# Kernel tuning notes

Hardware: AMD Instinct MI355X
Metric: run time of the kernel (lower is better)

## Reference

```python
import math
import jax, jax.numpy as jnp
import numpy as np

B = 128          # batch_size (graphs)
SEQ = 128        # max_seq_len (nodes per graph)
D = 128          # input_dim
HID = 64         # enc_hidden_dim
HEADS = 4        # in_head
N = B * SEQ      # total nodes
E = 262144       # edges (avg degree 16)


def _make_pe(seq, d):
    pos = np.arange(seq, dtype=np.float32)[:, None]
    i_even = np.arange(0, d, 2, dtype=np.float32)
    pe = np.zeros((seq, d), dtype=np.float32)
    pe[:, 0::2] = np.sin(pos / 10000.0 ** (2.0 * i_even / d))
    pe[:, 1::2] = np.cos(pos / 10000.0 ** (2.0 * (i_even + 1.0) / d))
    return jnp.asarray(pe)


def setup_inputs() -> dict:
    key = jax.random.key(0)
    ks = jax.random.split(key, 10)
    s = 0.1
    return {
        "x": jax.random.normal(ks[0], (N, D), jnp.float32),
        "edge_index": jax.random.randint(ks[1], (2, E), 0, N),
        "pe": _make_pe(SEQ, D),
        "W1": jax.random.normal(ks[2], (D, HEADS * HID), jnp.float32) * s,
        "a_src1": jax.random.normal(ks[3], (HEADS, HID), jnp.float32) * s,
        "a_dst1": jax.random.normal(ks[4], (HEADS, HID), jnp.float32) * s,
        "b1": jnp.zeros((HEADS * HID,), jnp.float32),
        "W2": jax.random.normal(ks[5], (HEADS * HID, HID), jnp.float32) * s,
        "a_src2": jax.random.normal(ks[6], (1, HID), jnp.float32) * s,
        "a_dst2": jax.random.normal(ks[7], (1, HID), jnp.float32) * s,
        "b2": jnp.zeros((HID,), jnp.float32),
        "batch_size": B,
    }


def _gat_conv(x, src, dst, W, a_src, a_dst, b, heads, ch, concat, n):
    # PyG GATConv (eval mode, self-loops already appended to src/dst).
    h = (x @ W).reshape(n, heads, ch)                      # [N,H,C]
    alpha_src = jnp.einsum("nhc,hc->nh", h, a_src)         # [N,H]
    alpha_dst = jnp.einsum("nhc,hc->nh", h, a_dst)
    e = jax.nn.leaky_relu(alpha_src[src] + alpha_dst[dst], 0.2)  # [E,H]
    m = jax.ops.segment_max(e, dst, num_segments=n)        # segment softmax over dst
    ex = jnp.exp(e - m[dst])
    den = jax.ops.segment_sum(ex, dst, num_segments=n)
    alpha = ex / (den[dst] + 1e-16)                        # [E,H]
    out = jax.ops.segment_sum(h[src] * alpha[:, :, None], dst, num_segments=n)
    out = out.reshape(n, heads * ch) if concat else out.mean(axis=1)
    return out + b


def reference(x, edge_index, pe, W1, a_src1, a_dst1, b1, W2, a_src2, a_dst2, b2, batch_size):
    n = x.shape[0]
    loop = jnp.arange(n)
    src = jnp.concatenate([edge_index[0], loop])           # add self-loops (PyG default)
    dst = jnp.concatenate([edge_index[1], loop])
    # positional encoding (dropout inactive in eval)
    h = x * math.sqrt(x.shape[1]) + jnp.tile(pe, (batch_size, 1))
    h = jax.nn.elu(_gat_conv(h, src, dst, W1, a_src1, a_dst1, b1, HEADS, HID, True, n))
    out = _gat_conv(h, src, dst, W2, a_src2, a_dst2, b2, 1, HID, False, n)
    return out.reshape(batch_size, -1, out.shape[1])
```

## Files before the change

### kernel.cpp

```cpp
#include <hip/hip_runtime.h>
#include <hip/hip_bf16.h>

typedef __hip_bfloat16 bf16;

#define N_NODES 16384
#define D_IN    128
#define HID     64
#define HEADS   4
#define F1      256
#define SEQ     128
#define SLOTS   64

__device__ __forceinline__ float wave_sum(float v) {
    #pragma unroll
    for (int o = 32; o > 0; o >>= 1) v += __shfl_xor(v, o, 64);
    return v;
}
__device__ __forceinline__ float lrelu(float v) { return v > 0.f ? v : 0.2f * v; }
__device__ __forceinline__ float rdlane(float v, int l) {
    return __uint_as_float(__builtin_amdgcn_readlane(__float_as_uint(v), l));
}

#define UNPACK8(u, te, acc)                                          \
    do {                                                             \
        acc[0] += (te) * __uint_as_float((u).x << 16);               \
        acc[1] += (te) * __uint_as_float((u).x & 0xffff0000u);       \
        acc[2] += (te) * __uint_as_float((u).y << 16);               \
        acc[3] += (te) * __uint_as_float((u).y & 0xffff0000u);       \
        acc[4] += (te) * __uint_as_float((u).z << 16);               \
        acc[5] += (te) * __uint_as_float((u).z & 0xffff0000u);       \
        acc[6] += (te) * __uint_as_float((u).w << 16);               \
        acc[7] += (te) * __uint_as_float((u).w & 0xffff0000u);       \
    } while (0)

__global__ __launch_bounds__(256) void k_gemm1s(const float* __restrict__ x,
                                                const float* __restrict__ pe,
                                                const float* __restrict__ W1,
                                                const float* __restrict__ a_src1,
                                                const float* __restrict__ a_dst1,
                                                bf16* __restrict__ h,
                                                float* __restrict__ as1,
                                                float* __restrict__ ad1,
                                                const int* __restrict__ ei, int E, int Etot,
                                                int* __restrict__ cnt,
                                                int* __restrict__ esrc) {
    __shared__ float4 ws[2048];
    int tid = threadIdx.x, lane = tid & 63, wv = tid >> 6;

    {
        int gtid = blockIdx.x * 256 + tid;
        for (int e = gtid; e < Etot; e += 262144) {
            int s, d;
            if (e < E) { s = ei[e]; d = ei[E + e]; }
            else       { s = e - E; d = s; }
            int pos = atomicAdd(&cnt[d], 1);
            if (pos < SLOTS) esrc[d * SLOTS + pos] = s;
        }
    }

    int base = blockIdx.x * 16;
    int j4 = lane * 4;
    float2 xr[4];
    #pragma unroll
    for (int i = 0; i < 4; i++) {
        int row = base + wv * 4 + i;
        float2 xa  = *(const float2*)(x  + (size_t)row * 128 + 2 * lane);
        float2 pea = *(const float2*)(pe + (size_t)(row & (SEQ - 1)) * 128 + 2 * lane);
        xr[i].x = xa.x * 11.313708499f + pea.x;
        xr[i].y = xa.y * 11.313708499f + pea.y;
    }
    float acc[4][4] = {};
    const float4* Wv = (const float4*)W1;
    for (int c = 0; c < 4; c++) {
        if (c > 0) __syncthreads();
        const float4* src = Wv + (size_t)c * 2048;
        #pragma unroll
        for (int i = 0; i < 8; i++) ws[i * 256 + tid] = src[i * 256 + tid];
        __syncthreads();
        #pragma unroll 4
        for (int lk2 = 0; lk2 < 16; lk2++) {
            int k2 = c * 16 + lk2;
            float4 w0 = ws[(2 * lk2) * 64 + lane];
            float4 w1 = ws[(2 * lk2 + 1) * 64 + lane];
            #pragma unroll
            for (int i = 0; i < 4; i++) {
                float a0 = rdlane(xr[i].x, k2);
                float a1 = rdlane(xr[i].y, k2);
                acc[i][0] += a0 * w0.x + a1 * w1.x;
                acc[i][1] += a0 * w0.y + a1 * w1.y;
                acc[i][2] += a0 * w0.z + a1 * w1.z;
                acc[i][3] += a0 * w0.w + a1 * w1.w;
            }
        }
    }
    float4 asv = *(const float4*)(a_src1 + j4);
    float4 adv = *(const float4*)(a_dst1 + j4);
    #pragma unroll
    for (int i = 0; i < 4; i++) {
        int row = base + wv * 4 + i;
        union { bf16 b[4]; ushort4 u; } cv;
        cv.b[0] = __float2bfloat16(acc[i][0]);
        cv.b[1] = __float2bfloat16(acc[i][1]);
        cv.b[2] = __float2bfloat16(acc[i][2]);
        cv.b[3] = __float2bfloat16(acc[i][3]);
        *(ushort4*)(h + (size_t)row * 256 + j4) = cv.u;
        float vs = acc[i][0] * asv.x + acc[i][1] * asv.y + acc[i][2] * asv.z + acc[i][3] * asv.w;
        float vd = acc[i][0] * adv.x + acc[i][1] * adv.y + acc[i][2] * adv.z + acc[i][3] * adv.w;
        #pragma unroll
        for (int o = 1; o < 16; o <<= 1) {
            vs += __shfl_xor(vs, o);
            vd += __shfl_xor(vd, o);
        }
        if ((lane & 15) == 0) {
            as1[row * 4 + (lane >> 4)] = vs;
            ad1[row * 4 + (lane >> 4)] = vd;
        }
    }
}

__global__ __launch_bounds__(256) void k_agg1_gemm2(
        const int* __restrict__ cnt, const int* __restrict__ esrc,
        const float* __restrict__ as1, const float* __restrict__ ad1,
        const bf16* __restrict__ h,
        const float* __restrict__ b1,
        const float* __restrict__ W2,
        const float* __restrict__ a_src2, const float* __restrict__ a_dst2,
        bf16* __restrict__ h2, float* __restrict__ as2, float* __restrict__ ad2) {
    __shared__ float hs[4][256];
    __shared__ float scr[1024];
    __shared__ int   ss[4][64];
    int tid = threadIdx.x, lane = tid & 63, wv = tid >> 6;
    int dbase = blockIdx.x * 4;
    int eg = lane >> 3;
    int cg_ = lane & 7;
    const bf16* hbase = h + (size_t)wv * 64 + cg_ * 8;

    int cv4 = cnt[dbase + (lane & 3)];

    #pragma unroll 4
    for (int it = 0; it < 4; it++) {
        int d = dbase + it;
        int deg = min(__shfl(cv4, it), SLOTS);
        int s = esrc[(size_t)d * SLOTS + lane] & (N_NODES - 1);
        float av = as1[(size_t)s * 4 + wv];
        float adw = ad1[d * 4 + wv];
        float t = (lane < deg) ? __expf(lrelu(av + adw) - 40.f) : 0.f;
        float inv = 1.f / wave_sum(t);
        scr[(it * 4 + wv) * 64 + lane] = t * inv;
        ss[it][lane] = s;
    }

    #pragma unroll 2
    for (int it = 0; it < 4; it++) {
        int deg = min(__shfl(cv4, it), SLOTS);
        const float* tsr = &scr[(it * 4 + wv) * 64];

        float acc[8] = {0, 0, 0, 0, 0, 0, 0, 0};
        if (4 * eg < deg) {
            int4   sv = *(const int4*)&ss[it][4 * eg];
            float4 tv = *(const float4*)(tsr + 4 * eg);
            uint4 u0 = *(const uint4*)(hbase + (size_t)sv.x * 256);
            uint4 u1 = *(const uint4*)(hbase + (size_t)sv.y * 256);
            uint4 u2 = *(const uint4*)(hbase + (size_t)sv.z * 256);
            uint4 u3 = *(const uint4*)(hbase + (size_t)sv.w * 256);
            UNPACK8(u0, tv.x, acc);
            UNPACK8(u1, tv.y, acc);
            UNPACK8(u2, tv.z, acc);
            UNPACK8(u3, tv.w, acc);
        }
        for (int sub = 32; sub < deg; sub += 32) {
            if (sub + 4 * eg < deg) {
                int4   s2 = *(const int4*)&ss[it][sub + 4 * eg];
                float4 t2 = *(const float4*)(tsr + sub + 4 * eg);
                uint4 u0 = *(const uint4*)(hbase + (size_t)s2.x * 256);
                uint4 u1 = *(const uint4*)(hbase + (size_t)s2.y * 256);
                uint4 u2 = *(const uint4*)(hbase + (size_t)s2.z * 256);
                uint4 u3 = *(const uint4*)(hbase + (size_t)s2.w * 256);
                UNPACK8(u0, t2.x, acc);
                UNPACK8(u1, t2.y, acc);
                UNPACK8(u2, t2.z, acc);
                UNPACK8(u3, t2.w, acc);
            }
        }
        #pragma unroll
        for (int j = 0; j < 8; j++) {
            acc[j] += __shfl_xor(acc[j], 8);
            acc[j] += __shfl_xor(acc[j], 16);
            acc[j] += __shfl_xor(acc[j], 32);
        }
        if (lane < 8) {
            int cbase = wv * 64 + lane * 8;
            const float4* b1v = (const float4*)(b1 + cbase);
            float4 bb0 = b1v[0], bb1 = b1v[1];
            float o[8];
            o[0] = acc[0] + bb0.x; o[1] = acc[1] + bb0.y;
            o[2] = acc[2] + bb0.z; o[3] = acc[3] + bb0.w;
            o[4] = acc[4] + bb1.x; o[5] = acc[5] + bb1.y;
            o[6] = acc[6] + bb1.z; o[7] = acc[7] + bb1.w;
            #pragma unroll
            for (int j = 0; j < 8; j++)
                o[j] = o[j] > 0.f ? o[j] : (__expf(o[j]) - 1.f);
            float4* dst = (float4*)&hs[it][cbase];
            dst[0] = make_float4(o[0], o[1], o[2], o[3]);
            dst[1] = make_float4(o[4], o[5], o[6], o[7]);
        }
    }
    __syncthreads();

    {
        float acc2[4] = {0, 0, 0, 0};
        const int k4base = wv * 16;
        for (int kk = 0; kk < 16; kk++) {
            int k4 = k4base + kk;
            const float* wp = W2 + (size_t)k4 * 256 + lane;
            float w0 = wp[0], w1 = wp[64], w2 = wp[128], w3 = wp[192];
            #pragma unroll
            for (int r = 0; r < 4; r++) {
                float4 u = *(const float4*)&hs[r][k4 * 4];
                acc2[r] += u.x * w0 + u.y * w1 + u.z * w2 + u.w * w3;
            }
        }
        #pragma unroll
        for (int r = 0; r < 4; r++) scr[(wv * 4 + r) * 64 + lane] = acc2[r];
    }
    __syncthreads();
    {
        int r = wv;
        float a0 = scr[(0 * 4 + r) * 64 + lane] + scr[(1 * 4 + r) * 64 + lane]
                 + scr[(2 * 4 + r) * 64 + lane] + scr[(3 * 4 + r) * 64 + lane];
        float asj = a_src2[lane], adj = a_dst2[lane];
        int n0 = dbase + r;
        h2[(size_t)n0 * 64 + lane] = __float2bfloat16(a0);
        float va0 = wave_sum(a0 * asj);
        float vd0 = wave_sum(a0 * adj);
        if (lane == 0) {
            as2[n0] = va0; ad2[n0] = vd0;
        }
    }
}

__global__ __launch_bounds__(256) void k_agg2(const int* __restrict__ cnt,
                                              const int* __restrict__ esrc,
                                              const float* __restrict__ as2,
                                              const float* __restrict__ ad2,
                                              const bf16* __restrict__ h2,
                                              const float* __restrict__ b2v,
                                              float* __restrict__ out) {
    __shared__ float ts[4][64];
    int tid = threadIdx.x, lane = tid & 63, wv = tid >> 6;
    int d = blockIdx.x * 4 + wv;
    int deg = min(cnt[d], SLOTS);
    int eg = lane >> 3, cg_ = lane & 7;
    const bf16* hbase = h2 + cg_ * 8;
    const int4* ep4 = (const int4*)(esrc + (size_t)d * SLOTS);

    int4 sv = ep4[eg];
    sv.x &= N_NODES - 1; sv.y &= N_NODES - 1;
    sv.z &= N_NODES - 1; sv.w &= N_NODES - 1;

    int s = esrc[(size_t)d * SLOTS + lane] & (N_NODES - 1);
    float av = as2[s];
    float adw = ad2[d];
    float t = (lane < deg) ? __expf(lrelu(av + adw) - 40.f) : 0.f;
    float inv = 1.f / wave_sum(t);
    ts[wv][lane] = t * inv;

    float acc[8] = {0, 0, 0, 0, 0, 0, 0, 0};
    if (4 * eg < deg) {
        uint4 u0 = *(const uint4*)(hbase + (size_t)sv.x * 64);
        uint4 u1 = *(const uint4*)(hbase + (size_t)sv.y * 64);
        uint4 u2 = *(const uint4*)(hbase + (size_t)sv.z * 64);
        uint4 u3 = *(const uint4*)(hbase + (size_t)sv.w * 64);
        float4 tv = *(const float4*)&ts[wv][4 * eg];
        UNPACK8(u0, tv.x, acc);
        UNPACK8(u1, tv.y, acc);
        UNPACK8(u2, tv.z, acc);
        UNPACK8(u3, tv.w, acc);
    }
    for (int sub = 32; sub < deg; sub += 32) {
        int4 s2 = ep4[(sub >> 2) + eg];
        s2.x &= N_NODES - 1; s2.y &= N_NODES - 1;
        s2.z &= N_NODES - 1; s2.w &= N_NODES - 1;
        if (sub + 4 * eg < deg) {
            uint4 u0 = *(const uint4*)(hbase + (size_t)s2.x * 64);
            uint4 u1 = *(const uint4*)(hbase + (size_t)s2.y * 64);
            uint4 u2 = *(const uint4*)(hbase + (size_t)s2.z * 64);
            uint4 u3 = *(const uint4*)(hbase + (size_t)s2.w * 64);
            float4 t2 = *(const float4*)&ts[wv][sub + 4 * eg];
            UNPACK8(u0, t2.x, acc);
            UNPACK8(u1, t2.y, acc);
            UNPACK8(u2, t2.z, acc);
            UNPACK8(u3, t2.w, acc);
        }
    }
    #pragma unroll
    for (int j = 0; j < 8; j++) {
        acc[j] += __shfl_xor(acc[j], 8);
        acc[j] += __shfl_xor(acc[j], 16);
        acc[j] += __shfl_xor(acc[j], 32);
    }
    if (lane < 8) {
        int cbase = lane * 8;
        float o[8];
        #pragma unroll
        for (int j = 0; j < 8; j++) o[j] = acc[j] + b2v[cbase + j];
        float4* dst = (float4*)(out + (size_t)d * 64 + cbase);
        dst[0] = make_float4(o[0], o[1], o[2], o[3]);
        dst[1] = make_float4(o[4], o[5], o[6], o[7]);
    }
}

extern "C" void kernel_launch(void* const* d_in, const int* in_sizes, int n_in,
                              void* d_out, int out_size, void* d_ws, size_t ws_size,
                              hipStream_t stream) {
    const float* x    = (const float*)d_in[0];
    const int*   ei   = (const int*)  d_in[1];
    const float* pe   = (const float*)d_in[2];
    const float* W1   = (const float*)d_in[3];
    const float* a_s1 = (const float*)d_in[4];
    const float* a_d1 = (const float*)d_in[5];
    const float* b1   = (const float*)d_in[6];
    const float* W2   = (const float*)d_in[7];
    const float* a_s2 = (const float*)d_in[8];
    const float* a_d2 = (const float*)d_in[9];
    const float* b2   = (const float*)d_in[10];

    const int E    = in_sizes[1] / 2;
    const int n    = N_NODES;
    const int Etot = E + n;

    char* p = (char*)d_ws;
    auto alloc = [&](size_t bytes) -> void* {
        void* r = (void*)p;
        p += (bytes + 255) & ~(size_t)255;
        return r;
    };
    int*   cnt     = (int*)  alloc((size_t)n * 4);
    int*   esrc    = (int*)  alloc((size_t)n * SLOTS * 4);
    bf16*  h       = (bf16*) alloc((size_t)n * F1 * 2);
    float* as1     = (float*)alloc((size_t)n * HEADS * 4);
    float* ad1     = (float*)alloc((size_t)n * HEADS * 4);
    bf16*  h2      = (bf16*) alloc((size_t)n * HID * 2);
    float* as2     = (float*)alloc((size_t)n * 4);
    float* ad2     = (float*)alloc((size_t)n * 4);

    hipMemsetAsync(cnt, 0, (size_t)n * 4, stream);

    k_gemm1s    <<<n / 16, 256, 0, stream>>>(x, pe, W1, a_s1, a_d1, h, as1, ad1,
                                             ei, E, Etot, cnt, esrc);
    k_agg1_gemm2<<<n / 4, 256, 0, stream>>>(cnt, esrc, as1, ad1, h, b1,
                                            W2, a_s2, a_d2, h2, as2, ad2);
    k_agg2      <<<n / 4, 256, 0, stream>>>(cnt, esrc, as2, ad2, h2, b2, (float*)d_out);
}
```

Baseline: 170.8 us.

## Switch GAT aggregation to lane-per-channel gathers with packed src/weight pairs in LDS

Both aggregation kernels are restructured. Previously 8 edge groups each loaded 16-byte bf16 vectors and combined results with a cross-lane shuffle reduction. Now each lane owns one channel and walks the edge list serially, loading one bf16 per edge with the next loads prefetched ahead. Source indices and softmax weights are packed as int2 in shared memory so one ds read yields both, and the shuffle reductions plus lane<8 writeback are removed. The trade is many narrow 2-byte gathers in a serial per-wave loop instead of wide parallel vector loads, which could hurt memory efficiency.

```diff
diff --git a/kernel.cpp b/kernel.cpp
--- a/kernel.cpp
+++ b/kernel.cpp
@@ -20,18 +20,9 @@
 __device__ __forceinline__ float rdlane(float v, int l) {
     return __uint_as_float(__builtin_amdgcn_readlane(__float_as_uint(v), l));
 }
-
-#define UNPACK8(u, te, acc)                                          \
-    do {                                                             \
-        acc[0] += (te) * __uint_as_float((u).x << 16);               \
-        acc[1] += (te) * __uint_as_float((u).x & 0xffff0000u);       \
-        acc[2] += (te) * __uint_as_float((u).y << 16);               \
-        acc[3] += (te) * __uint_as_float((u).y & 0xffff0000u);       \
-        acc[4] += (te) * __uint_as_float((u).z << 16);               \
-        acc[5] += (te) * __uint_as_float((u).z & 0xffff0000u);       \
-        acc[6] += (te) * __uint_as_float((u).w << 16);               \
-        acc[7] += (te) * __uint_as_float((u).w & 0xffff0000u);       \
-    } while (0)
+__device__ __forceinline__ float bfu(unsigned short u) {
+    return __uint_as_float((unsigned)u << 16);
+}
 
 __global__ __launch_bounds__(256) void k_gemm1s(const float* __restrict__ x,
                                                 const float* __restrict__ pe,
@@ -127,17 +118,13 @@
         const float* __restrict__ a_src2, const float* __restrict__ a_dst2,
         bf16* __restrict__ h2, float* __restrict__ as2, float* __restrict__ ad2) {
     __shared__ float hs[4][256];
-    __shared__ float scr[1024];
-    __shared__ int   ss[4][64];
+    __shared__ int2  sts[16][64];
     int tid = threadIdx.x, lane = tid & 63, wv = tid >> 6;
     int dbase = blockIdx.x * 4;
-    int eg = lane >> 3;
-    int cg_ = lane & 7;
-    const bf16* hbase = h + (size_t)wv * 64 + cg_ * 8;
 
     int cv4 = cnt[dbase + (lane & 3)];
 
-    #pragma unroll 4
+    #pragma unroll
     for (int it = 0; it < 4; it++) {
         int d = dbase + it;
         int deg = min(__shfl(cv4, it), SLOTS);
@@ -146,66 +133,47 @@
         float adw = ad1[d * 4 + wv];
         float t = (lane < deg) ? __expf(lrelu(av + adw) - 40.f) : 0.f;
         float inv = 1.f / wave_sum(t);
-        scr[(it * 4 + wv) * 64 + lane] = t * inv;
-        ss[it][lane] = s;
-    }
-
+        int2 pr; pr.x = s; pr.y = __float_as_int(t * inv);
+        sts[it * 4 + wv][lane] = pr;
+    }
+
+    const unsigned short* hb = (const unsigned short*)h + (size_t)wv * 64 + lane;
+    float bb = b1[wv * 64 + lane];
     #pragma unroll 2
     for (int it = 0; it < 4; it++) {
         int deg = min(__shfl(cv4, it), SLOTS);
-        const float* tsr = &scr[(it * 4 + wv) * 64];
-
-        float acc[8] = {0, 0, 0, 0, 0, 0, 0, 0};
-        if (4 * eg < deg) {
-            int4   sv = *(const int4*)&ss[it][4 * eg];
-            float4 tv = *(const float4*)(tsr + 4 * eg);
-            uint4 u0 = *(const uint4*)(hbase + (size_t)sv.x * 256);
-            uint4 u1 = *(const uint4*)(hbase + (size_t)sv.y * 256);
-            uint4 u2 = *(const uint4*)(hbase + (size_t)sv.z * 256);
-            uint4 u3 = *(const uint4*)(hbase + (size_t)sv.w * 256);
-            UNPACK8(u0, tv.x, acc);
-            UNPACK8(u1, tv.y, acc);
-            UNPACK8(u2, tv.z, acc);
-            UNPACK8(u3, tv.w, acc);
-        }
-        for (int sub = 32; sub < deg; sub += 32) {
-            if (sub + 4 * eg < deg) {
-                int4   s2 = *(const int4*)&ss[it][sub + 4 * eg];
-                float4 t2 = *(const float4*)(tsr + sub + 4 * eg);
-                uint4 u0 = *(const uint4*)(hbase + (size_t)s2.x * 256);
-                uint4 u1 = *(const uint4*)(hbase + (size_t)s2.y * 256);
-                uint4 u2 = *(const uint4*)(hbase + (size_t)s2.z * 256);
-                uint4 u3 = *(const uint4*)(hbase + (size_t)s2.w * 256);
-                UNPACK8(u0, t2.x, acc);
-                UNPACK8(u1, t2.y, acc);
-                UNPACK8(u2, t2.z, acc);
-                UNPACK8(u3, t2.w, acc);
-            }
-        }
-        #pragma unroll
-        for (int j = 0; j < 8; j++) {
-            acc[j] += __shfl_xor(acc[j], 8);
-            acc[j] += __shfl_xor(acc[j], 16);
-            acc[j] += __shfl_xor(acc[j], 32);
-        }
-        if (lane < 8) {
-            int cbase = wv * 64 + lane * 8;
-            const float4* b1v = (const float4*)(b1 + cbase);
-            float4 bb0 = b1v[0], bb1 = b1v[1];
-            float o[8];
-            o[0] = acc[0] + bb0.x; o[1] = acc[1] + bb0.y;
-            o[2] = acc[2] + bb0.z; o[3] = acc[3] + bb0.w;
-            o[4] = acc[4] + bb1.x; o[5] = acc[5] + bb1.y;
-            o[6] = acc[6] + bb1.z; o[7] = acc[7] + bb1.w;
-            #pragma unroll
-            for (int j = 0; j < 8; j++)
-                o[j] = o[j] > 0.f ? o[j] : (__expf(o[j]) - 1.f);
-            float4* dst = (float4*)&hs[it][cbase];
-            dst[0] = make_float4(o[0], o[1], o[2], o[3]);
-            dst[1] = make_float4(o[4], o[5], o[6], o[7]);
-        }
+        const int4* row4 = (const int4*)sts[it * 4 + wv];
+        int nq = (deg + 3) >> 2;
+        float acc = 0.f;
+        int4 A = row4[0];
+        int4 B = row4[1];
+        unsigned short e0 = hb[(size_t)A.x * 256];
+        unsigned short e1 = hb[(size_t)A.z * 256];
+        unsigned short e2 = hb[(size_t)B.x * 256];
+        unsigned short e3 = hb[(size_t)B.z * 256];
+        for (int q = 1; q < nq; q++) {
+            int4 An = row4[2 * q];
+            int4 Bn = row4[2 * q + 1];
+            unsigned short f0 = hb[(size_t)An.x * 256];
+            unsigned short f1 = hb[(size_t)An.z * 256];
+            unsigned short f2 = hb[(size_t)Bn.x * 256];
+            unsigned short f3 = hb[(size_t)Bn.z * 256];
+            acc += bfu(e0) * __uint_as_float(A.y);
+            acc += bfu(e1) * __uint_as_float(A.w);
+            acc += bfu(e2) * __uint_as_float(B.y);
+            acc += bfu(e3) * __uint_as_float(B.w);
+            A = An; B = Bn; e0 = f0; e1 = f1; e2 = f2; e3 = f3;
+        }
+        acc += bfu(e0) * __uint_as_float(A.y);
+        acc += bfu(e1) * __uint_as_float(A.w);
+        acc += bfu(e2) * __uint_as_float(B.y);
+        acc += bfu(e3) * __uint_as_float(B.w);
+        float v = acc + bb;
+        hs[it][wv * 64 + lane] = v > 0.f ? v : (__expf(v) - 1.f);
     }
     __syncthreads();
+
+    float* part = (float*)sts;
 
     {
         float acc2[4] = {0, 0, 0, 0};
@@ -221,13 +189,13 @@
             }
         }
         #pragma unroll
-        for (int r = 0; r < 4; r++) scr[(wv * 4 + r) * 64 + lane] = acc2[r];
+        for (int r = 0; r < 4; r++) part[(wv * 4 + r) * 64 + lane] = acc2[r];
     }
     __syncthreads();
     {
         int r = wv;
-        float a0 = scr[(0 * 4 + r) * 64 + lane] + scr[(1 * 4 + r) * 64 + lane]
-                 + scr[(2 * 4 + r) * 64 + lane] + scr[(3 * 4 + r) * 64 + lane];
+        float a0 = part[(0 * 4 + r) * 64 + lane] + part[(1 * 4 + r) * 64 + lane]
+                 + part[(2 * 4 + r) * 64 + lane] + part[(3 * 4 + r) * 64 + lane];
         float asj = a_src2[lane], adj = a_dst2[lane];
         int n0 = dbase + r;
         h2[(size_t)n0 * 64 + lane] = __float2bfloat16(a0);
@@ -246,68 +214,47 @@
                                               const bf16* __restrict__ h2,
                                               const float* __restrict__ b2v,
                                               float* __restrict__ out) {
-    __shared__ float ts[4][64];
+    __shared__ int2 sts2[4][64];
     int tid = threadIdx.x, lane = tid & 63, wv = tid >> 6;
     int d = blockIdx.x * 4 + wv;
     int deg = min(cnt[d], SLOTS);
-    int eg = lane >> 3, cg_ = lane & 7;
-    const bf16* hbase = h2 + cg_ * 8;
-    const int4* ep4 = (const int4*)(esrc + (size_t)d * SLOTS);
-
-    int4 sv = ep4[eg];
-    sv.x &= N_NODES - 1; sv.y &= N_NODES - 1;
-    sv.z &= N_NODES - 1; sv.w &= N_NODES - 1;
 
     int s = esrc[(size_t)d * SLOTS + lane] & (N_NODES - 1);
     float av = as2[s];
     float adw = ad2[d];
     float t = (lane < deg) ? __expf(lrelu(av + adw) - 40.f) : 0.f;
     float inv = 1.f / wave_sum(t);
-    ts[wv][lane] = t * inv;
-
-    float acc[8] = {0, 0, 0, 0, 0, 0, 0, 0};
-    if (4 * eg < deg) {
-        uint4 u0 = *(const uint4*)(hbase + (size_t)sv.x * 64);
-        uint4 u1 = *(const uint4*)(hbase + (size_t)sv.y * 64);
-        uint4 u2 = *(const uint4*)(hbase + (size_t)sv.z * 64);
-        uint4 u3 = *(const uint4*)(hbase + (size_t)sv.w * 64);
-        float4 tv = *(const float4*)&ts[wv][4 * eg];
-        UNPACK8(u0, tv.x, acc);
-        UNPACK8(u1, tv.y, acc);
-        UNPACK8(u2, tv.z, acc);
-        UNPACK8(u3, tv.w, acc);
-    }
-    for (int sub = 32; sub < deg; sub += 32) {
-        int4 s2 = ep4[(sub >> 2) + eg];
-        s2.x &= N_NODES - 1; s2.y &= N_NODES - 1;
-        s2.z &= N_NODES - 1; s2.w &= N_NODES - 1;
-        if (sub + 4 * eg < deg) {
-            uint4 u0 = *(const uint4*)(hbase + (size_t)s2.x * 64);
-            uint4 u1 = *(const uint4*)(hbase + (size_t)s2.y * 64);
-            uint4 u2 = *(const uint4*)(hbase + (size_t)s2.z * 64);
-            uint4 u3 = *(const uint4*)(hbase + (size_t)s2.w * 64);
-            float4 t2 = *(const float4*)&ts[wv][sub + 4 * eg];
-            UNPACK8(u0, t2.x, acc);
-            UNPACK8(u1, t2.y, acc);
-            UNPACK8(u2, t2.z, acc);
-            UNPACK8(u3, t2.w, acc);
-        }
-    }
-    #pragma unroll
-    for (int j = 0; j < 8; j++) {
-        acc[j] += __shfl_xor(acc[j], 8);
-        acc[j] += __shfl_xor(acc[j], 16);
-        acc[j] += __shfl_xor(acc[j], 32);
-    }
-    if (lane < 8) {
-        int cbase = lane * 8;
-        float o[8];
-        #pragma unroll
-        for (int j = 0; j < 8; j++) o[j] = acc[j] + b2v[cbase + j];
-        float4* dst = (float4*)(out + (size_t)d * 64 + cbase);
-        dst[0] = make_float4(o[0], o[1], o[2], o[3]);
-        dst[1] = make_float4(o[4], o[5], o[6], o[7]);
-    }
+    int2 pr; pr.x = s; pr.y = __float_as_int(t * inv);
+    sts2[wv][lane] = pr;
+
+    const unsigned short* hb = (const unsigned short*)h2 + lane;
+    const int4* row4 = (const int4*)sts2[wv];
+    int nq = (deg + 3) >> 2;
+    float acc = 0.f;
+    int4 A = row4[0];
+    int4 B = row4[1];
+    unsigned short e0 = hb[(size_t)A.x * 64];
+    unsigned short e1 = hb[(size_t)A.z * 64];
+    unsigned short e2 = hb[(size_t)B.x * 64];
+    unsigned short e3 = hb[(size_t)B.z * 64];
+    for (int q = 1; q < nq; q++) {
+        int4 An = row4[2 * q];
+        int4 Bn = row4[2 * q + 1];
+        unsigned short f0 = hb[(size_t)An.x * 64];
+        unsigned short f1 = hb[(size_t)An.z * 64];
+        unsigned short f2 = hb[(size_t)Bn.x * 64];
+        unsigned short f3 = hb[(size_t)Bn.z * 64];
+        acc += bfu(e0) * __uint_as_float(A.y);
+        acc += bfu(e1) * __uint_as_float(A.w);
+        acc += bfu(e2) * __uint_as_float(B.y);
+        acc += bfu(e3) * __uint_as_float(B.w);
+        A = An; B = Bn; e0 = f0; e1 = f1; e2 = f2; e3 = f3;
+    }
+    acc += bfu(e0) * __uint_as_float(A.y);
+    acc += bfu(e1) * __uint_as_float(A.w);
+    acc += bfu(e2) * __uint_as_float(B.y);
+    acc += bfu(e3) * __uint_as_float(B.w);
+    out[(size_t)d * 64 + lane] = acc + b2v[lane];
 }
 
 extern "C" void kernel_launch(void* const* d_in, const int* in_sizes, int n_in,
```

New measurement: 166.9 us. -2.3%, faster.
